# Performance work log

Hardware: AMD Instinct MI355X
Metric: run time of the kernel (lower is better)

Reference implementation:

```python
import jax, jax.numpy as jnp
import numpy as np

NUM_VECTORS = 8192
DIM = 64

def setup_inputs() -> dict:
    key = jax.random.key(0)
    kx, kw = jax.random.split(key)
    x = jax.random.normal(kx, (8, 4096, DIM), dtype=jnp.float32)
    W = jax.random.normal(kw, (NUM_VECTORS, DIM), dtype=jnp.float32)
    return {"x": x, "W": W}

def reference(x, W):
    # x: [B, S, C] channels_last (ndim==3 -> channels_first=False)
    shape = x.shape
    flat = x.reshape(-1, shape[-1])  # [N, C]
    # cdist + argmin: argmin of squared euclidean distance is identical to argmin of cdist
    x2 = jnp.sum(flat * flat, axis=1, keepdims=True)          # [N, 1]
    w2 = jnp.sum(W * W, axis=1)                                # [K]
    d2 = x2 - 2.0 * (flat @ W.T) + w2                          # [N, K] dominant intermediate
    indices = jnp.argmin(d2, axis=1)                           # [N]
    z = W[indices]                                             # gather [N, C]
    # losses (use_ema=True -> codebook_loss = 0)
    commitment_loss = jnp.mean((z - jax.lax.stop_gradient(flat)) ** 2)
    codebook_loss = jnp.zeros_like(commitment_loss)
    # straight-through estimator
    z_st = flat + jax.lax.stop_gradient(z - flat)
    # perplexity: scatter one-hot counts -> mean -> entropy
    n = flat.shape[0]
    counts = jnp.zeros((NUM_VECTORS,), dtype=jnp.float32).at[indices].add(1.0)
    avg_probs = counts / n
    perplexity = jnp.exp(-jnp.sum(avg_probs * jnp.log(avg_probs + 1e-10)))
    z_out = z_st.reshape(shape)
    return (z_out, codebook_loss, commitment_loss, perplexity)
```

## Files before the change

kernel.cpp:

```cpp
#include <hip/hip_runtime.h>
#include <math.h>

#define N_ROWS 32768
#define K_CODES 8192
#define DIM 64
#define CHUNKS 4
#define CPC (K_CODES / CHUNKS)
#define TILES (CPC / 32)

using half8  = __attribute__((ext_vector_type(8))) _Float16;
using f32x16 = __attribute__((ext_vector_type(16))) float;

#define WS_W2     0
#define WS_COUNTS 32768
#define WS_CSUM   65536
#define WS_BEST   65552
#define WS_WHL    327936

__device__ __forceinline__ void gload_lds16(const _Float16* g, _Float16* l) {
    __builtin_amdgcn_global_load_lds(
        (const __attribute__((address_space(1))) void*)g,
        (__attribute__((address_space(3))) void*)l, 16, 0, 0);
}

__global__ __launch_bounds__(256) void vq_prep(const float* __restrict__ W,
                                               _Float16* __restrict__ whl,
                                               float* __restrict__ w2g,
                                               unsigned long long* __restrict__ best,
                                               int* __restrict__ counts,
                                               float* __restrict__ csum) {
    int g = blockIdx.x * 256 + threadIdx.x;
    int code = g >> 6, k = g & 63;
    float w = W[g];
    _Float16 h  = (_Float16)w;
    _Float16 lo = (_Float16)(w - (float)h);
    whl[(size_t)code * 128 + k]      = h;
    whl[(size_t)code * 128 + 64 + k] = lo;
    float s = w * w;
    #pragma unroll
    for (int off = 32; off; off >>= 1) s += __shfl_down(s, off);
    if (k == 0) w2g[code] = s;
    if (g < N_ROWS)  best[g] = ~0ULL;
    if (g < K_CODES) counts[g] = 0;
    if (g == 0)      *csum = 0.f;
}

__global__ __launch_bounds__(256, 4) void vq_mfma(const float* __restrict__ x,
                                                  const _Float16* __restrict__ whl,
                                                  const float* __restrict__ w2g,
                                                  unsigned long long* __restrict__ best) {
    __shared__ __align__(16) _Float16 lds[2][4096];

    const int t     = threadIdx.x;
    const int wv    = t >> 6;
    const int l     = t & 63;
    const int ln31  = l & 31;
    const int lhalf = l >> 5;
    const int chunk = blockIdx.x & (CHUNKS - 1);
    const int rblk  = blockIdx.x / CHUNKS;
    const int rowb  = rblk * 128 + wv * 32;
    const int cbase = chunk * CPC;

    half8 ahi[4], alo[4];
    {
        const float* xr = x + (size_t)(rowb + ln31) * DIM + lhalf * 8;
        #pragma unroll
        for (int kt = 0; kt < 4; ++kt) {
            float4 a0 = *(const float4*)(xr + kt * 16);
            float4 a1 = *(const float4*)(xr + kt * 16 + 4);
            float fa[8] = {a0.x, a0.y, a0.z, a0.w, a1.x, a1.y, a1.z, a1.w};
            #pragma unroll
            for (int j = 0; j < 8; ++j) {
                _Float16 h = (_Float16)fa[j];
                ahi[kt][j] = h;
                alo[kt][j] = (_Float16)(fa[j] - (float)h);
            }
        }
    }

    const _Float16* srcp[2];
    int ldsG[2];
    #pragma unroll
    for (int p = 0; p < 2; ++p) {
        int q = p * 4 + wv;
        srcp[p] = whl + (size_t)(cbase + ln31) * 128 + ((q & 1) * 8 + lhalf + 2 * (q >> 1)) * 8;
        ldsG[p] = (p * 256 + wv * 64) * 8;
    }

    float bv[16];
    int   bi[16];
    #pragma unroll
    for (int s2 = 0; s2 < 16; ++s2) { bv[s2] = 3.4e38f; bi[s2] = 0; }

    #pragma unroll
    for (int p = 0; p < 2; ++p) gload_lds16(srcp[p], &lds[0][0] + ldsG[p]);
    __syncthreads();

    const float* w2p = w2g + cbase + ln31;
    int cur = 0;

    for (int tile = 0; tile < TILES; ++tile) {
        if (tile < TILES - 1) {
            #pragma unroll
            for (int p = 0; p < 2; ++p)
                gload_lds16(srcp[p] + (tile + 1) * 4096, &lds[0][0] + (cur ^ 1) * 4096 + ldsG[p]);
        }
        const float w2v = w2p[tile * 32];
        const _Float16* lb = &lds[0][0] + cur * 4096;

        f32x16 acc = {};
        __builtin_amdgcn_s_setprio(1);
        #pragma unroll
        for (int kt = 0; kt < 4; ++kt) {
            half8 bh = *(const half8*)(lb + ((kt * 2 + 0) * 64 + l) * 8);
            half8 bl = *(const half8*)(lb + ((kt * 2 + 1) * 64 + l) * 8);
            acc = __builtin_amdgcn_mfma_f32_32x32x16_f16(ahi[kt], bh, acc, 0, 0, 0);
            acc = __builtin_amdgcn_mfma_f32_32x32x16_f16(alo[kt], bh, acc, 0, 0, 0);
            acc = __builtin_amdgcn_mfma_f32_32x32x16_f16(ahi[kt], bl, acc, 0, 0, 0);
        }
        __builtin_amdgcn_s_setprio(0);

        const int cc = cbase + tile * 32 + ln31;
        #pragma unroll
        for (int s2 = 0; s2 < 16; ++s2) {
            float sA = fmaf(-2.f, acc[s2], w2v);
            if (sA < bv[s2]) { bv[s2] = sA; bi[s2] = cc; }
        }
        __syncthreads();
        cur ^= 1;
    }

    #pragma unroll
    for (int s2 = 0; s2 < 16; ++s2) {
        unsigned uk = __float_as_uint(bv[s2]);
        uk = (uk >> 31) ? ~uk : (uk | 0x80000000u);
        unsigned long long key = ((unsigned long long)uk << 32) | (unsigned)bi[s2];
        #pragma unroll
        for (int off = 16; off; off >>= 1) {
            unsigned long long o = __shfl_xor(key, off);
            key = (o < key) ? o : key;
        }
        if (ln31 == 0) {
            int rl = (s2 & 3) + 8 * (s2 >> 2) + 4 * lhalf;
            atomicMin(&best[rowb + rl], key);
        }
    }
}

__global__ __launch_bounds__(256) void vq_gather(const float* __restrict__ x,
                                                 const float* __restrict__ W,
                                                 const unsigned long long* __restrict__ best,
                                                 float* __restrict__ zout,
                                                 int* __restrict__ counts,
                                                 float* __restrict__ csum) {
    int t   = threadIdx.x;
    int row = blockIdx.x * 64 + (t >> 2);
    int seg = t & 3;
    int idx = (int)(best[row] & 0xFFFFFFFFULL);
    if (seg == 0) atomicAdd(&counts[idx], 1);
    const float* wrow = W    + (size_t)idx * DIM + seg * 16;
    const float* xrow = x    + (size_t)row * DIM + seg * 16;
    float*       zrow = zout + (size_t)row * DIM + seg * 16;
    float local = 0.f;
    #pragma unroll
    for (int j = 0; j < 16; j += 4) {
        float4 wv = *(const float4*)(wrow + j);
        float4 xv = *(const float4*)(xrow + j);
        *(float4*)(zrow + j) = wv;
        float dx = wv.x - xv.x, dy = wv.y - xv.y, dz = wv.z - xv.z, dw = wv.w - xv.w;
        local += dx * dx + dy * dy + dz * dz + dw * dw;
    }
    #pragma unroll
    for (int off = 32; off; off >>= 1) local += __shfl_down(local, off);
    if ((t & 63) == 0) atomicAdd(csum, local);
}

__global__ __launch_bounds__(256) void vq_final(const int* __restrict__ counts,
                                                const float* __restrict__ csum,
                                                float* __restrict__ out3) {
    __shared__ float sh[4];
    float e = 0.f;
    for (int i = threadIdx.x; i < K_CODES; i += 256) {
        float p = (float)counts[i] * (1.0f / N_ROWS);
        e += p * logf(p + 1e-10f);
    }
    #pragma unroll
    for (int off = 32; off; off >>= 1) e += __shfl_down(e, off);
    if ((threadIdx.x & 63) == 0) sh[threadIdx.x >> 6] = e;
    __syncthreads();
    if (threadIdx.x == 0) {
        float tot = sh[0] + sh[1] + sh[2] + sh[3];
        out3[0] = 0.f;
        out3[1] = csum[0] * (1.0f / ((float)N_ROWS * DIM));
        out3[2] = expf(-tot);
    }
}

extern "C" void kernel_launch(void* const* d_in, const int* in_sizes, int n_in,
                              void* d_out, int out_size, void* d_ws, size_t ws_size,
                              hipStream_t stream) {
    (void)in_sizes; (void)n_in; (void)out_size; (void)ws_size;
    const float* x = (const float*)d_in[0];
    const float* W = (const float*)d_in[1];
    float* zout = (float*)d_out;
    float* out3 = (float*)d_out + (size_t)N_ROWS * DIM;

    float*              w2g    = (float*)((char*)d_ws + WS_W2);
    int*                counts = (int*)((char*)d_ws + WS_COUNTS);
    float*              csum   = (float*)((char*)d_ws + WS_CSUM);
    unsigned long long* best   = (unsigned long long*)((char*)d_ws + WS_BEST);
    _Float16*           whl    = (_Float16*)((char*)d_ws + WS_WHL);

    vq_prep  <<<K_CODES * DIM / 256,     256, 0, stream>>>(W, whl, w2g, best, counts, csum);
    vq_mfma  <<<(N_ROWS / 128) * CHUNKS, 256, 0, stream>>>(x, whl, w2g, best);
    vq_gather<<<N_ROWS / 64,             256, 0, stream>>>(x, W, best, zout, counts, csum);
    vq_final <<<1,                       256, 0, stream>>>(counts, csum, out3);
}
```

Before: 156.4 us.

## Derive commitment loss from best distance key and split MFMA accumulators

```diff
diff --git a/kernel.cpp b/kernel.cpp
--- a/kernel.cpp
+++ b/kernel.cpp
@@ -15,7 +15,8 @@
 #define WS_COUNTS 32768
 #define WS_CSUM   65536
 #define WS_BEST   65552
-#define WS_WHL    327936
+#define WS_X2     327696
+#define WS_WHL    458768
 
 __device__ __forceinline__ void gload_lds16(const _Float16* g, _Float16* l) {
     __builtin_amdgcn_global_load_lds(
@@ -24,8 +25,10 @@
 }
 
 __global__ __launch_bounds__(256) void vq_prep(const float* __restrict__ W,
+                                               const float* __restrict__ x,
                                                _Float16* __restrict__ whl,
                                                float* __restrict__ w2g,
+                                               float* __restrict__ x2g,
                                                unsigned long long* __restrict__ best,
                                                int* __restrict__ counts,
                                                float* __restrict__ csum) {
@@ -40,6 +43,11 @@
     #pragma unroll
     for (int off = 32; off; off >>= 1) s += __shfl_down(s, off);
     if (k == 0) w2g[code] = s;
+    float4 xv = *(const float4*)(x + (size_t)g * 4);
+    float ss = xv.x * xv.x + xv.y * xv.y + xv.z * xv.z + xv.w * xv.w;
+    #pragma unroll
+    for (int off = 8; off; off >>= 1) ss += __shfl_down(ss, off);
+    if ((g & 15) == 0) x2g[g >> 4] = ss;
     if (g < N_ROWS)  best[g] = ~0ULL;
     if (g < K_CODES) counts[g] = 0;
     if (g == 0)      *csum = 0.f;
@@ -50,6 +58,7 @@
                                                   const float* __restrict__ w2g,
                                                   unsigned long long* __restrict__ best) {
     __shared__ __align__(16) _Float16 lds[2][4096];
+    __shared__ float w2l[CPC];
 
     const int t     = threadIdx.x;
     const int wv    = t >> 6;
@@ -60,6 +69,8 @@
     const int rblk  = blockIdx.x / CHUNKS;
     const int rowb  = rblk * 128 + wv * 32;
     const int cbase = chunk * CPC;
+
+    for (int i = t; i < CPC; i += 256) w2l[i] = w2g[cbase + i];
 
     half8 ahi[4], alo[4];
     {
@@ -96,34 +107,32 @@
     for (int p = 0; p < 2; ++p) gload_lds16(srcp[p], &lds[0][0] + ldsG[p]);
     __syncthreads();
 
-    const float* w2p = w2g + cbase + ln31;
     int cur = 0;
-
     for (int tile = 0; tile < TILES; ++tile) {
         if (tile < TILES - 1) {
             #pragma unroll
             for (int p = 0; p < 2; ++p)
                 gload_lds16(srcp[p] + (tile + 1) * 4096, &lds[0][0] + (cur ^ 1) * 4096 + ldsG[p]);
         }
-        const float w2v = w2p[tile * 32];
+        const float w2v = w2l[tile * 32 + ln31];
         const _Float16* lb = &lds[0][0] + cur * 4096;
 
-        f32x16 acc = {};
+        f32x16 accA = {}, accB = {};
         __builtin_amdgcn_s_setprio(1);
         #pragma unroll
         for (int kt = 0; kt < 4; ++kt) {
             half8 bh = *(const half8*)(lb + ((kt * 2 + 0) * 64 + l) * 8);
             half8 bl = *(const half8*)(lb + ((kt * 2 + 1) * 64 + l) * 8);
-            acc = __builtin_amdgcn_mfma_f32_32x32x16_f16(ahi[kt], bh, acc, 0, 0, 0);
-            acc = __builtin_amdgcn_mfma_f32_32x32x16_f16(alo[kt], bh, acc, 0, 0, 0);
-            acc = __builtin_amdgcn_mfma_f32_32x32x16_f16(ahi[kt], bl, acc, 0, 0, 0);
+            accA = __builtin_amdgcn_mfma_f32_32x32x16_f16(ahi[kt], bh, accA, 0, 0, 0);
+            accB = __builtin_amdgcn_mfma_f32_32x32x16_f16(alo[kt], bh, accB, 0, 0, 0);
+            accB = __builtin_amdgcn_mfma_f32_32x32x16_f16(ahi[kt], bl, accB, 0, 0, 0);
         }
         __builtin_amdgcn_s_setprio(0);
 
         const int cc = cbase + tile * 32 + ln31;
         #pragma unroll
         for (int s2 = 0; s2 < 16; ++s2) {
-            float sA = fmaf(-2.f, acc[s2], w2v);
+            float sA = fmaf(-2.f, accA[s2], fmaf(-2.f, accB[s2], w2v));
             if (sA < bv[s2]) { bv[s2] = sA; bi[s2] = cc; }
         }
         __syncthreads();
@@ -147,28 +156,29 @@
     }
 }
 
-__global__ __launch_bounds__(256) void vq_gather(const float* __restrict__ x,
-                                                 const float* __restrict__ W,
+__global__ __launch_bounds__(256) void vq_gather(const float* __restrict__ W,
                                                  const unsigned long long* __restrict__ best,
+                                                 const float* __restrict__ x2g,
                                                  float* __restrict__ zout,
                                                  int* __restrict__ counts,
                                                  float* __restrict__ csum) {
     int t   = threadIdx.x;
     int row = blockIdx.x * 64 + (t >> 2);
     int seg = t & 3;
-    int idx = (int)(best[row] & 0xFFFFFFFFULL);
-    if (seg == 0) atomicAdd(&counts[idx], 1);
+    unsigned long long key = best[row];
+    int idx = (int)(key & 0xFFFFFFFFULL);
+
     const float* wrow = W    + (size_t)idx * DIM + seg * 16;
-    const float* xrow = x    + (size_t)row * DIM + seg * 16;
     float*       zrow = zout + (size_t)row * DIM + seg * 16;
+    #pragma unroll
+    for (int j = 0; j < 16; j += 4) *(float4*)(zrow + j) = *(const float4*)(wrow + j);
+
     float local = 0.f;
-    #pragma unroll
-    for (int j = 0; j < 16; j += 4) {
-        float4 wv = *(const float4*)(wrow + j);
-        float4 xv = *(const float4*)(xrow + j);
-        *(float4*)(zrow + j) = wv;
-        float dx = wv.x - xv.x, dy = wv.y - xv.y, dz = wv.z - xv.z, dw = wv.w - xv.w;
-        local += dx * dx + dy * dy + dz * dz + dw * dw;
+    if (seg == 0) {
+        atomicAdd(&counts[idx], 1);
+        unsigned uk = (unsigned)(key >> 32);
+        unsigned ob = (uk & 0x80000000u) ? (uk & 0x7FFFFFFFu) : ~uk;
+        local = x2g[row] + __uint_as_float(ob);
     }
     #pragma unroll
     for (int off = 32; off; off >>= 1) local += __shfl_down(local, off);
@@ -209,10 +219,11 @@
     int*                counts = (int*)((char*)d_ws + WS_COUNTS);
     float*              csum   = (float*)((char*)d_ws + WS_CSUM);
     unsigned long long* best   = (unsigned long long*)((char*)d_ws + WS_BEST);
+    float*              x2g    = (float*)((char*)d_ws + WS_X2);
     _Float16*           whl    = (_Float16*)((char*)d_ws + WS_WHL);
 
-    vq_prep  <<<K_CODES * DIM / 256,     256, 0, stream>>>(W, whl, w2g, best, counts, csum);
+    vq_prep  <<<K_CODES * DIM / 256,     256, 0, stream>>>(W, x, whl, w2g, x2g, best, counts, csum);
     vq_mfma  <<<(N_ROWS / 128) * CHUNKS, 256, 0, stream>>>(x, whl, w2g, best);
-    vq_gather<<<N_ROWS / 64,             256, 0, stream>>>(x, W, best, zout, counts, csum);
+    vq_gather<<<N_ROWS / 64,             256, 0, stream>>>(W, best, x2g, zout, counts, csum);
     vq_final <<<1,                       256, 0, stream>>>(counts, csum, out3);
 }
```

Measured after the change: 160.7 us. 1.03x slower.
